# Kernel optimization log

Hardware: AMD Instinct MI355X
Metric: run time of the kernel (lower is better)

## Reference

```python
import jax, jax.numpy as jnp
import numpy as np

B = 8; A = 9; NUM_CLASSES = 80
BRANCH_HW = [(80, 80), (40, 40)]; STRIDES = [8, 16]
IMG_H, IMG_W = 640, 640
CLASS_OFFSETS = [0, 0]
SCORE_THR = 0.05; NMS_THR = 0.5; MARGIN = 0.0
PRE_NMS = 1000; POST_NMS = 300
MIN_H, MIN_W = 0.0, 0.0
BBOX_CLIP = float(np.log(1000.0 / 16.0))  # torchvision-style dw/dh clamp


def _make_anchors(H, W, stride):
    # A square anchors per cell, grid-aligned (x1,y1,x2,y2)
    sizes = np.array([16., 32., 64., 20., 40., 80., 24., 48., 96.])[:A]
    cx = (np.arange(W) + 0.5) * stride
    cy = (np.arange(H) + 0.5) * stride
    cy_g, cx_g = np.meshgrid(cy, cx, indexing='ij')  # [H,W]
    half = sizes / 2.0  # [A]
    x1 = cx_g[..., None] - half; y1 = cy_g[..., None] - half
    x2 = cx_g[..., None] + half; y2 = cy_g[..., None] + half
    anc = np.stack([x1, y1, x2, y2], -1).astype(np.float32)  # [H,W,A,4]
    anc = anc.reshape(H, W, A * 4).transpose(2, 0, 1)  # [A*4,H,W]
    return jnp.asarray(np.broadcast_to(anc[None], (B,) + anc.shape).copy())


def setup_inputs() -> dict:
    key = jax.random.key(0)
    ks = jax.random.split(key, 2)
    out = {}
    for i, (Hh, Ww) in enumerate(BRANCH_HW):
        d = jax.random.normal(ks[i], (B, Hh, Ww, A, 4 + NUM_CLASSES), jnp.float32)
        d = d.at[..., :4].multiply(0.25)  # keep box deltas in a sane range
        out['data%d' % i] = d.reshape(B, Hh, Ww, A * (4 + NUM_CLASSES)).transpose(0, 3, 1, 2)
        out['anchors%d' % i] = _make_anchors(Hh, Ww, STRIDES[i])
    return out


def _unfold(t, d):
    b = t.shape[0]
    return jnp.transpose(t, (0, 2, 3, 1)).reshape(b, -1, d)


def _decode(deltas, anchors):
    # BoxCoder((1,1,1,1)).decode_single
    aw = anchors[..., 2] - anchors[..., 0]; ah = anchors[..., 3] - anchors[..., 1]
    acx = anchors[..., 0] + 0.5 * aw; acy = anchors[..., 1] + 0.5 * ah
    dx, dy, dw, dh = (deltas[..., 0], deltas[..., 1], deltas[..., 2], deltas[..., 3])
    pcx = dx * aw + acx; pcy = dy * ah + acy
    pw = jnp.exp(jnp.minimum(dw, BBOX_CLIP)) * aw
    ph = jnp.exp(jnp.minimum(dh, BBOX_CLIP)) * ah
    return jnp.stack([pcx - 0.5 * pw, pcy - 0.5 * ph, pcx + 0.5 * pw, pcy + 0.5 * ph], -1)


def _iou(b):
    area = (b[:, 2] - b[:, 0]) * (b[:, 3] - b[:, 1])
    lt = jnp.maximum(b[:, None, :2], b[None, :, :2])
    rb = jnp.minimum(b[:, None, 2:], b[None, :, 2:])
    wh = jnp.clip(rb - lt, 0.0)
    inter = wh[..., 0] * wh[..., 1]
    return inter / (area[:, None] + area[None, :] - inter + 1e-9)


def _nms_single(boxes, cls, scores):
    # sort by score, take pre_nms_top_k
    sc, idx = jax.lax.top_k(scores, PRE_NMS)
    b = boxes[idx]; c = cls[idx]
    # score threshold + min-hw validity filter (masked instead of dynamic slice)
    valid = (sc >= SCORE_THR) & (b[:, 0] < b[:, 2] - MIN_W) & (b[:, 1] < b[:, 3] - MIN_H)
    iou = _iou(b)  # [PRE,PRE]
    rng = jnp.arange(PRE_NMS)

    def body(i, keep):
        # box j suppressed by kept box i if IoU>thr and score_i - score_j > margin
        sup = keep[i] & (iou[i] > NMS_THR) & ((sc[i] - sc) > MARGIN) & (rng > i)
        return keep & (~sup)

    keep = jax.lax.fori_loop(0, PRE_NMS, body, valid)
    # kept boxes first (score order preserved), then pad_zero to POST_NMS
    order = jnp.argsort(jnp.where(keep, rng, rng + PRE_NMS))[:POST_NMS]
    km = keep[order]
    return (jnp.where(km[:, None], b[order], 0.0),
            jnp.where(km, sc[order], 0.0),
            jnp.where(km, c[order], 0.0))


def reference(data0, data1, anchors0, anchors1):
    datas = [data0, data1]; ancs = [anchors0, anchors1]
    fa, deltas, scores, offs = [], [], [], []
    for i in range(2):
        fa.append(_unfold(ancs[i], 4))
        u = _unfold(datas[i], 4 + NUM_CLASSES)
        deltas.append(u[..., :4]); scores.append(u[..., 4:])
        offs.append(jnp.full((1, u.shape[1]), float(CLASS_OFFSETS[i]), jnp.float32))
    fa = jnp.concatenate(fa, 1); deltas = jnp.concatenate(deltas, 1)
    scores = jnp.concatenate(scores, 1); offs = jnp.concatenate(offs, 1)
    max_sc = scores.max(-1)
    cls = jnp.argmax(scores, -1).astype(jnp.float32) + offs
    boxes = _decode(deltas, fa)
    # clip to image
    x = jnp.clip(boxes[..., 0::2], 0.0, float(IMG_W))
    y = jnp.clip(boxes[..., 1::2], 0.0, float(IMG_H))
    boxes = jnp.stack([x[..., 0], y[..., 0], x[..., 1], y[..., 1]], -1)
    return jax.vmap(_nms_single)(boxes, cls, max_sc)  # ([B,POST,4],[B,POST],[B,POST])
```

## Files before the change

### kernel.cpp

```cpp
#include <hip/hip_runtime.h>
#include <math.h>

#pragma clang fp contract(off)

#define BB      8
#define AA      9
#define NCLS    80
#define NTOT    72000
#define PRE     1000
#define POST    300
#define CAP     4096
#define BCLIP   4.135166556742356f

__device__ __constant__ float c_sizes[9] = {16.f,32.f,64.f,20.f,40.f,80.f,24.f,48.f,96.f};

__device__ inline unsigned fkey(float s) {
    unsigned u = __float_as_uint(s);
    return (u & 0x80000000u) ? ~u : (u | 0x80000000u);
}

template<int BR>
__device__ inline void fused_impl(int bx, const float* __restrict__ data,
    float* __restrict__ boxes, float* __restrict__ scores, float* __restrict__ cls,
    unsigned* __restrict__ chist, unsigned* lh)
{
    constexpr int ROWF4  = BR ? 400 : 1600;
    constexpr int W      = BR ? 40 : 80;
    constexpr int STRIDE = BR ? 16 : 8;
    constexpr int NQ     = BR ? 2 : 8;

    int slab = bx / NQ;
    int q    = bx - slab * NQ;
    int b = slab / 9, a = slab - (slab / 9) * 9;
    int tid = threadIdx.x;
    bool act = tid < 200;

    const float4* d4 = (const float4*)data;
    size_t rowbase = (size_t)(b * 756 + a * 84) * ROWF4 + q * 200;

    if (act) {
        float4 del[4];
        #pragma unroll
        for (int u = 0; u < 4; u++)
            del[u] = d4[rowbase + (size_t)u * ROWF4 + tid];

        float best[4];
        int   bc[4];
        #pragma unroll
        for (int k = 0; k < 4; k++) { best[k] = -INFINITY; bc[k] = 0; }

        for (int c0 = 4; c0 < 84; c0 += 8) {
            float4 v[8];
            #pragma unroll
            for (int u = 0; u < 8; u++)
                v[u] = d4[rowbase + (size_t)(c0 + u) * ROWF4 + tid];
            #pragma unroll
            for (int u = 0; u < 8; u++) {
                int c = c0 + u - 4;
                float s0[4];
                *(float4*)s0 = v[u];
                #pragma unroll
                for (int k = 0; k < 4; k++)
                    if (s0[k] > best[k]) { best[k] = s0[k]; bc[k] = c; }
            }
        }

        float sz = c_sizes[a];
        float dx[4], dy[4], dwv[4], dhv[4];
        *(float4*)dx  = del[0];
        *(float4*)dy  = del[1];
        *(float4*)dwv = del[2];
        *(float4*)dhv = del[3];

        int ml0 = q * 800 + tid * 4;
        size_t obase = (size_t)b * NTOT + (BR ? (57600 + a * 1600) : (a * 6400));

        #pragma unroll
        for (int k = 0; k < 4; k++) {
            int hw = ml0 + k;
            int h = hw / W, w = hw - h * W;
            float cy = (h + 0.5f) * (float)STRIDE;
            float cx = (w + 0.5f) * (float)STRIDE;
            float pcx = dx[k] * sz + cx;
            float pcy = dy[k] * sz + cy;
            float pw  = expf(fminf(dwv[k], BCLIP)) * sz;
            float ph  = expf(fminf(dhv[k], BCLIP)) * sz;
            float x1 = fminf(fmaxf(pcx - 0.5f * pw, 0.f), 640.f);
            float y1 = fminf(fmaxf(pcy - 0.5f * ph, 0.f), 640.f);
            float x2 = fminf(fmaxf(pcx + 0.5f * pw, 0.f), 640.f);
            float y2 = fminf(fmaxf(pcy + 0.5f * ph, 0.f), 640.f);
            size_t o = obase + hw;
            ((float4*)boxes)[o] = make_float4(x1, y1, x2, y2);
            scores[o] = best[k];
            cls[o]    = (float)bc[k];
            atomicAdd(&lh[fkey(best[k]) >> 24], 1u);
        }
    }
    __syncthreads();
    if (lh[tid]) atomicAdd(&chist[b * 256 + tid], lh[tid]);
}

__global__ __launch_bounds__(256) void k_fused(
    const float* __restrict__ data0, const float* __restrict__ data1,
    float* __restrict__ boxes, float* __restrict__ scores, float* __restrict__ cls,
    unsigned* __restrict__ chist)
{
    __shared__ unsigned lh[256];
    lh[threadIdx.x] = 0;
    __syncthreads();
    int bx = blockIdx.x;
    if (bx < 576) fused_impl<0>(bx, data0, boxes, scores, cls, chist, lh);
    else          fused_impl<1>(bx - 576, data1, boxes, scores, cls, chist, lh);
}

__global__ __launch_bounds__(256) void k_fine(const float* __restrict__ scores,
                                              const unsigned* __restrict__ chist,
                                              unsigned* __restrict__ fhist)
{
    __shared__ unsigned S[256];
    __shared__ unsigned lh[256];
    __shared__ unsigned sC;
    int tid = threadIdx.x, b = blockIdx.y;
    S[tid]  = chist[b * 256 + tid];
    lh[tid] = 0;
    __syncthreads();
    for (int off = 1; off < 256; off <<= 1) {
        unsigned v = S[tid] + ((tid + off < 256) ? S[tid + off] : 0u);
        __syncthreads();
        S[tid] = v;
        __syncthreads();
    }
    if (S[tid] >= (unsigned)PRE && (tid == 255 || S[tid + 1] < (unsigned)PRE)) sC = tid;
    __syncthreads();
    unsigned C = sC;

    int m4 = blockIdx.x * 256 + tid;
    if (m4 < NTOT / 4) {
        float sv[4];
        *(float4*)sv = ((const float4*)(scores + (size_t)b * NTOT))[m4];
        #pragma unroll
        for (int k = 0; k < 4; k++) {
            unsigned u = fkey(sv[k]);
            if ((u >> 24) == C) atomicAdd(&lh[(u >> 16) & 0xFF], 1u);
        }
    }
    __syncthreads();
    if (lh[tid]) atomicAdd(&fhist[b * 256 + tid], lh[tid]);
}

__global__ __launch_bounds__(256) void k_compact(const float* __restrict__ scores,
                                                 const unsigned* __restrict__ chist,
                                                 const unsigned* __restrict__ fhist,
                                                 unsigned* __restrict__ cnt,
                                                 unsigned long long* __restrict__ cand)
{
    __shared__ unsigned S[256];
    __shared__ unsigned sC, sCa, sT;
    int tid = threadIdx.x, b = blockIdx.y;

    S[tid] = chist[b * 256 + tid];
    __syncthreads();
    for (int off = 1; off < 256; off <<= 1) {
        unsigned v = S[tid] + ((tid + off < 256) ? S[tid + off] : 0u);
        __syncthreads();
        S[tid] = v;
        __syncthreads();
    }
    if (S[tid] >= (unsigned)PRE && (tid == 255 || S[tid + 1] < (unsigned)PRE)) {
        sC  = tid;
        sCa = (tid == 255) ? 0u : S[tid + 1];
    }
    __syncthreads();
    unsigned C = sC, ca = sCa;
    S[tid] = fhist[b * 256 + tid];
    __syncthreads();
    for (int off = 1; off < 256; off <<= 1) {
        unsigned v = S[tid] + ((tid + off < 256) ? S[tid + off] : 0u);
        __syncthreads();
        S[tid] = v;
        __syncthreads();
    }
    if (ca + S[tid] >= (unsigned)PRE && (tid == 255 || ca + S[tid + 1] < (unsigned)PRE))
        sT = (C << 8) | (unsigned)tid;
    __syncthreads();
    unsigned Tb = sT;

    int m4 = blockIdx.x * 256 + tid;
    if (m4 >= NTOT / 4) return;
    float sv[4];
    *(float4*)sv = ((const float4*)(scores + (size_t)b * NTOT))[m4];
    #pragma unroll
    for (int k = 0; k < 4; k++) {
        unsigned u = fkey(sv[k]);
        if ((u >> 16) >= Tb) {
            int m = m4 * 4 + k;
            int n;
            if (m < 57600) { int a = m / 6400; int hw = m - a * 6400; n = hw * 9 + a; }
            else { int mm = m - 57600; int a = mm / 1600; int hw = mm - a * 1600; n = 57600 + hw * 9 + a; }
            unsigned pos = atomicAdd(&cnt[b], 1u);
            if (pos < CAP)
                cand[(size_t)b * CAP + pos] = ((unsigned long long)u << 32) | (unsigned)(~(unsigned)n);
        }
    }
}

__global__ __launch_bounds__(1024) void k_sort(
    const unsigned long long* __restrict__ cand, const unsigned* __restrict__ cnt,
    const float* __restrict__ boxes, const float* __restrict__ scores, const float* __restrict__ cls,
    float* __restrict__ sboxes, float* __restrict__ sscores, float* __restrict__ scls)
{
    __shared__ unsigned long long keys[CAP];
    int b = blockIdx.x, tid = threadIdx.x;
    int c = min((int)cnt[b], CAP);
    int P = 1024;
    while (P < c) P <<= 1;
    for (int i = tid; i < P; i += 1024)
        keys[i] = (i < c) ? cand[(size_t)b * CAP + i] : 0ULL;

    for (int k2 = 2; k2 <= P; k2 <<= 1)
        for (int j = k2 >> 1; j > 0; j >>= 1) {
            __syncthreads();
            for (int i = tid; i < P; i += 1024) {
                int l = i ^ j;
                if (l > i) {
                    unsigned long long x = keys[i], y = keys[l];
                    bool up = ((i & k2) == 0);
                    if ((x > y) == up) { keys[i] = y; keys[l] = x; }
                }
            }
        }
    __syncthreads();

    if (tid < PRE) {
        unsigned long long key = keys[P - 1 - tid];
        int n = (int)~(unsigned)(key & 0xFFFFFFFFu);
        int m;
        if (n < 57600) { int hw = n / 9; int a = n - hw * 9; m = a * 6400 + hw; }
        else { int n2 = n - 57600; int hw = n2 / 9; int a = n2 - hw * 9; m = 57600 + a * 1600 + hw; }
        size_t src = (size_t)b * NTOT + m;
        ((float4*)sboxes)[b * 1024 + tid] = ((const float4*)boxes)[src];
        sscores[b * 1024 + tid] = scores[src];
        scls[b * 1024 + tid] = cls[src];
    }
}

__global__ __launch_bounds__(1024) void k_mask(const float* __restrict__ sboxes,
                                               const float* __restrict__ sscores,
                                               unsigned long long* __restrict__ maskT)
{
    __shared__ float4 bx[64];
    __shared__ float  sl[64];
    int b = blockIdx.y, w = blockIdx.x, tid = threadIdx.x;
    if (tid < 64) {
        int i = w * 64 + tid;
        bx[tid] = ((const float4*)sboxes)[b * 1024 + i];
        sl[tid] = sscores[b * 1024 + i];
    }
    __syncthreads();
    int j = tid;
    unsigned long long* dst = &maskT[((size_t)(b * 16) + w) * 1024 + j];
    if (j >= PRE || w * 64 >= j) { *dst = 0ULL; return; }

    float4 bj = ((const float4*)sboxes)[b * 1024 + j];
    float sj = sscores[b * 1024 + j];
    float areaj = (bj.z - bj.x) * (bj.w - bj.y);
    unsigned long long bits = 0;
    int iend = min(64, j - w * 64);
    for (int ii = 0; ii < iend; ii++) {
        float4 bi = bx[ii];
        float ix1 = fmaxf(bi.x, bj.x), iy1 = fmaxf(bi.y, bj.y);
        float ix2 = fminf(bi.z, bj.z), iy2 = fminf(bi.w, bj.w);
        float iw = fmaxf(ix2 - ix1, 0.f), ih = fmaxf(iy2 - iy1, 0.f);
        float inter = iw * ih;
        float areai = (bi.z - bi.x) * (bi.w - bi.y);
        float iou = inter / (areai + areaj - inter + 1e-9f);
        if (iou > 0.5f && sl[ii] > sj) bits |= 1ull << ii;
    }
    *dst = bits;
}

__global__ __launch_bounds__(64) void k_nms(const unsigned long long* __restrict__ maskT,
                                            const float* __restrict__ sboxes,
                                            const float* __restrict__ sscores,
                                            const float* __restrict__ scls,
                                            float* __restrict__ out)
{
    int b = blockIdx.x, lane = threadIdx.x;
    const unsigned long long* base = maskT + (size_t)b * 16 * 1024;

    unsigned validbits = 0;
    #pragma unroll
    for (int c = 0; c < 16; c++) {
        int r = c * 64 + lane;
        bool v = false;
        if (r < PRE) {
            float sc = sscores[b * 1024 + r];
            float4 bbx = ((const float4*)sboxes)[b * 1024 + r];
            v = (sc >= 0.05f) && (bbx.x < bbx.z) && (bbx.y < bbx.w);
        }
        validbits |= (v ? 1u : 0u) << c;
    }

    unsigned long long keptw[16];
    #pragma unroll
    for (int c = 0; c < 16; c++) {
        unsigned long long acc = 0, col = 0;
        #pragma unroll
        for (int w = 0; w <= c; w++) {
            unsigned long long m = base[(w << 10) + c * 64 + lane];
            if (w < c) acc |= m & keptw[w];
            else       col = m;
        }
        bool alive = (((validbits >> c) & 1u) != 0u) && (acc == 0ULL);

        unsigned long long ab = __ballot(alive);
        unsigned long long kw = 0;
        while (ab) {
            int f = __ffsll((unsigned long long)ab) - 1;
            kw |= 1ULL << f;
            alive = alive && (lane != f) && (((col >> f) & 1ULL) == 0ULL);
            ab = __ballot(alive);
        }
        keptw[c] = kw;
    }

    __shared__ unsigned long long kws[16];
    __shared__ int pfx[17];
    if (lane == 0) {
        int s = 0;
        #pragma unroll
        for (int w = 0; w < 16; w++) {
            kws[w] = keptw[w];
            pfx[w] = s;
            s += __popcll(keptw[w]);
        }
        pfx[16] = s;
    }
    __syncthreads();
    int nk = pfx[16];

    float* ob = out;
    float* os = out + BB * POST * 4;
    float* oc = os + BB * POST;

    for (int r = lane; r < PRE; r += 64) {
        int w = r >> 6;
        unsigned long long kw = kws[w];
        if ((kw >> (r & 63)) & 1ULL) {
            int rank = pfx[w] + __popcll(kw & ((1ULL << (r & 63)) - 1ULL));
            if (rank < POST) {
                ((float4*)ob)[b * POST + rank] = ((const float4*)sboxes)[b * 1024 + r];
                os[b * POST + rank] = sscores[b * 1024 + r];
                oc[b * POST + rank] = scls[b * 1024 + r];
            }
        }
    }
    for (int p = nk + lane; p < POST; p += 64) {
        ((float4*)ob)[b * POST + p] = make_float4(0.f, 0.f, 0.f, 0.f);
        os[b * POST + p] = 0.f;
        oc[b * POST + p] = 0.f;
    }
}

extern "C" void kernel_launch(void* const* d_in, const int* in_sizes, int n_in,
                              void* d_out, int out_size, void* d_ws, size_t ws_size,
                              hipStream_t stream)
{
    const float* data0 = (const float*)d_in[0];
    const float* data1 = (const float*)d_in[2];
    for (int i = 0; i < n_in; i++) {
        if (in_sizes[i] == 8 * 756 * 6400) data0 = (const float*)d_in[i];
        else if (in_sizes[i] == 8 * 756 * 1600) data1 = (const float*)d_in[i];
    }

    char* ws = (char*)d_ws;
    size_t off = 0;
    auto alloc = [&](size_t bytes) -> char* {
        char* p = ws + off;
        off = (off + bytes + 255) & ~(size_t)255;
        return p;
    };

    float* boxes   = (float*)alloc((size_t)BB * NTOT * 4 * 4);
    float* scores  = (float*)alloc((size_t)BB * NTOT * 4);
    float* cls     = (float*)alloc((size_t)BB * NTOT * 4);
    unsigned* cnt   = (unsigned*)alloc(BB * 4);
    unsigned* chist = (unsigned*)alloc(BB * 256 * 4);
    unsigned* fhist = (unsigned*)alloc(BB * 256 * 4);
    unsigned long long* cand = (unsigned long long*)alloc((size_t)BB * CAP * 8);
    float* sboxes  = (float*)alloc((size_t)BB * 1024 * 4 * 4);
    float* sscores = (float*)alloc((size_t)BB * 1024 * 4);
    float* scls    = (float*)alloc((size_t)BB * 1024 * 4);
    unsigned long long* maskT = (unsigned long long*)alloc((size_t)BB * 16 * 1024 * 8);

    (void)hipMemsetAsync(cnt, 0, 256 + 2 * (size_t)BB * 256 * 4, stream);

    k_fused<<<720, 256, 0, stream>>>(data0, data1, boxes, scores, cls, chist);

    dim3 gf((NTOT / 4 + 255) / 256, BB);
    k_fine<<<gf, 256, 0, stream>>>(scores, chist, fhist);

    k_compact<<<gf, 256, 0, stream>>>(scores, chist, fhist, cnt, cand);

    k_sort<<<BB, 1024, 0, stream>>>(cand, cnt, boxes, scores, cls, sboxes, sscores, scls);

    dim3 g5(16, BB);
    k_mask<<<g5, 1024, 0, stream>>>(sboxes, sscores, maskT);

    k_nms<<<BB, 64, 0, stream>>>(maskT, sboxes, sscores, scls, (float*)d_out);
}
```

Baseline: 438.6 us.

## Decode boxes only for selected candidates and fuse sort, mask and NMS kernels

Box decoding is removed from the full-map pass and done only for the top-1000 candidates, reading deltas straight from the input tensors. The two-pass radix histogram becomes a single 16-bit global histogram built in the fused pass, with a small threshold kernel replacing the fine-histogram pass over all scores. The sort, IoU mask and NMS kernels are merged into one per-batch block that keeps boxes in shared memory. This cuts full-size box writes, one full score rescan and several launches, at the cost of a larger global histogram with contended atomics, a larger memset, and only 8 blocks doing the mask computation.

```diff
diff --git a/kernel.cpp b/kernel.cpp
--- a/kernel.cpp
+++ b/kernel.cpp
@@ -18,111 +18,82 @@
     unsigned u = __float_as_uint(s);
     return (u & 0x80000000u) ? ~u : (u | 0x80000000u);
 }
+__device__ inline float unfkey(unsigned u) {
+    return __uint_as_float((u & 0x80000000u) ? (u ^ 0x80000000u) : ~u);
+}
 
 template<int BR>
 __device__ inline void fused_impl(int bx, const float* __restrict__ data,
-    float* __restrict__ boxes, float* __restrict__ scores, float* __restrict__ cls,
-    unsigned* __restrict__ chist, unsigned* lh)
+    float* __restrict__ scores, float* __restrict__ cls,
+    unsigned* __restrict__ fhist16)
 {
     constexpr int ROWF4  = BR ? 400 : 1600;
-    constexpr int W      = BR ? 40 : 80;
-    constexpr int STRIDE = BR ? 16 : 8;
     constexpr int NQ     = BR ? 2 : 8;
 
     int slab = bx / NQ;
     int q    = bx - slab * NQ;
     int b = slab / 9, a = slab - (slab / 9) * 9;
     int tid = threadIdx.x;
-    bool act = tid < 200;
+    if (tid >= 200) return;
 
     const float4* d4 = (const float4*)data;
     size_t rowbase = (size_t)(b * 756 + a * 84) * ROWF4 + q * 200;
 
-    if (act) {
-        float4 del[4];
-        #pragma unroll
-        for (int u = 0; u < 4; u++)
-            del[u] = d4[rowbase + (size_t)u * ROWF4 + tid];
-
-        float best[4];
-        int   bc[4];
-        #pragma unroll
-        for (int k = 0; k < 4; k++) { best[k] = -INFINITY; bc[k] = 0; }
-
-        for (int c0 = 4; c0 < 84; c0 += 8) {
-            float4 v[8];
+    float best[4];
+    int   bc[4];
+    #pragma unroll
+    for (int k = 0; k < 4; k++) { best[k] = -INFINITY; bc[k] = 0; }
+
+    for (int c0 = 4; c0 < 84; c0 += 8) {
+        float4 v[8];
+        #pragma unroll
+        for (int u = 0; u < 8; u++)
+            v[u] = d4[rowbase + (size_t)(c0 + u) * ROWF4 + tid];
+        #pragma unroll
+        for (int u = 0; u < 8; u++) {
+            int c = c0 + u - 4;
+            float s0[4];
+            *(float4*)s0 = v[u];
             #pragma unroll
-            for (int u = 0; u < 8; u++)
-                v[u] = d4[rowbase + (size_t)(c0 + u) * ROWF4 + tid];
-            #pragma unroll
-            for (int u = 0; u < 8; u++) {
-                int c = c0 + u - 4;
-                float s0[4];
-                *(float4*)s0 = v[u];
-                #pragma unroll
-                for (int k = 0; k < 4; k++)
-                    if (s0[k] > best[k]) { best[k] = s0[k]; bc[k] = c; }
-            }
-        }
-
-        float sz = c_sizes[a];
-        float dx[4], dy[4], dwv[4], dhv[4];
-        *(float4*)dx  = del[0];
-        *(float4*)dy  = del[1];
-        *(float4*)dwv = del[2];
-        *(float4*)dhv = del[3];
-
-        int ml0 = q * 800 + tid * 4;
-        size_t obase = (size_t)b * NTOT + (BR ? (57600 + a * 1600) : (a * 6400));
-
-        #pragma unroll
-        for (int k = 0; k < 4; k++) {
-            int hw = ml0 + k;
-            int h = hw / W, w = hw - h * W;
-            float cy = (h + 0.5f) * (float)STRIDE;
-            float cx = (w + 0.5f) * (float)STRIDE;
-            float pcx = dx[k] * sz + cx;
-            float pcy = dy[k] * sz + cy;
-            float pw  = expf(fminf(dwv[k], BCLIP)) * sz;
-            float ph  = expf(fminf(dhv[k], BCLIP)) * sz;
-            float x1 = fminf(fmaxf(pcx - 0.5f * pw, 0.f), 640.f);
-            float y1 = fminf(fmaxf(pcy - 0.5f * ph, 0.f), 640.f);
-            float x2 = fminf(fmaxf(pcx + 0.5f * pw, 0.f), 640.f);
-            float y2 = fminf(fmaxf(pcy + 0.5f * ph, 0.f), 640.f);
-            size_t o = obase + hw;
-            ((float4*)boxes)[o] = make_float4(x1, y1, x2, y2);
-            scores[o] = best[k];
-            cls[o]    = (float)bc[k];
-            atomicAdd(&lh[fkey(best[k]) >> 24], 1u);
-        }
-    }
-    __syncthreads();
-    if (lh[tid]) atomicAdd(&chist[b * 256 + tid], lh[tid]);
+            for (int k = 0; k < 4; k++)
+                if (s0[k] > best[k]) { best[k] = s0[k]; bc[k] = c; }
+        }
+    }
+
+    int ml0 = q * 800 + tid * 4;
+    size_t obase = (size_t)b * NTOT + (BR ? (57600 + a * 1600) : (a * 6400));
+    size_t o4 = (obase + ml0) >> 2;
+    ((float4*)scores)[o4] = make_float4(best[0], best[1], best[2], best[3]);
+    ((float4*)cls)[o4]    = make_float4((float)bc[0], (float)bc[1],
+                                        (float)bc[2], (float)bc[3]);
+    unsigned* hb = fhist16 + (size_t)b * 65536;
+    #pragma unroll
+    for (int k = 0; k < 4; k++)
+        atomicAdd(&hb[fkey(best[k]) >> 16], 1u);
 }
 
 __global__ __launch_bounds__(256) void k_fused(
     const float* __restrict__ data0, const float* __restrict__ data1,
-    float* __restrict__ boxes, float* __restrict__ scores, float* __restrict__ cls,
-    unsigned* __restrict__ chist)
-{
-    __shared__ unsigned lh[256];
-    lh[threadIdx.x] = 0;
-    __syncthreads();
+    float* __restrict__ scores, float* __restrict__ cls,
+    unsigned* __restrict__ fhist16)
+{
     int bx = blockIdx.x;
-    if (bx < 576) fused_impl<0>(bx, data0, boxes, scores, cls, chist, lh);
-    else          fused_impl<1>(bx - 576, data1, boxes, scores, cls, chist, lh);
-}
-
-__global__ __launch_bounds__(256) void k_fine(const float* __restrict__ scores,
-                                              const unsigned* __restrict__ chist,
-                                              unsigned* __restrict__ fhist)
+    if (bx < 576) fused_impl<0>(bx, data0, scores, cls, fhist16);
+    else          fused_impl<1>(bx - 576, data1, scores, cls, fhist16);
+}
+
+__global__ __launch_bounds__(256) void k_thr(const unsigned* __restrict__ fhist16,
+                                             unsigned* __restrict__ T)
 {
     __shared__ unsigned S[256];
-    __shared__ unsigned lh[256];
-    __shared__ unsigned sC;
-    int tid = threadIdx.x, b = blockIdx.y;
-    S[tid]  = chist[b * 256 + tid];
-    lh[tid] = 0;
+    __shared__ unsigned sC, sCa;
+    int b = blockIdx.x, tid = threadIdx.x;
+
+    const uint4* h4 = (const uint4*)(fhist16 + (size_t)b * 65536 + tid * 256);
+    unsigned s = 0;
+    #pragma unroll 8
+    for (int i = 0; i < 64; i++) { uint4 v = h4[i]; s += v.x + v.y + v.z + v.w; }
+    S[tid] = s;
     __syncthreads();
     for (int off = 1; off < 256; off <<= 1) {
         unsigned v = S[tid] + ((tid + off < 256) ? S[tid + off] : 0u);
@@ -130,35 +101,14 @@
         S[tid] = v;
         __syncthreads();
     }
-    if (S[tid] >= (unsigned)PRE && (tid == 255 || S[tid + 1] < (unsigned)PRE)) sC = tid;
-    __syncthreads();
-    unsigned C = sC;
-
-    int m4 = blockIdx.x * 256 + tid;
-    if (m4 < NTOT / 4) {
-        float sv[4];
-        *(float4*)sv = ((const float4*)(scores + (size_t)b * NTOT))[m4];
-        #pragma unroll
-        for (int k = 0; k < 4; k++) {
-            unsigned u = fkey(sv[k]);
-            if ((u >> 24) == C) atomicAdd(&lh[(u >> 16) & 0xFF], 1u);
-        }
-    }
-    __syncthreads();
-    if (lh[tid]) atomicAdd(&fhist[b * 256 + tid], lh[tid]);
-}
-
-__global__ __launch_bounds__(256) void k_compact(const float* __restrict__ scores,
-                                                 const unsigned* __restrict__ chist,
-                                                 const unsigned* __restrict__ fhist,
-                                                 unsigned* __restrict__ cnt,
-                                                 unsigned long long* __restrict__ cand)
-{
-    __shared__ unsigned S[256];
-    __shared__ unsigned sC, sCa, sT;
-    int tid = threadIdx.x, b = blockIdx.y;
-
-    S[tid] = chist[b * 256 + tid];
+    if (S[tid] >= (unsigned)PRE && (tid == 255 || S[tid + 1] < (unsigned)PRE)) {
+        sC  = tid;
+        sCa = (tid == 255) ? 0u : S[tid + 1];
+    }
+    __syncthreads();
+    unsigned C = sC, ca = sCa;
+
+    S[tid] = fhist16[(size_t)b * 65536 + C * 256 + tid];
     __syncthreads();
     for (int off = 1; off < 256; off <<= 1) {
         unsigned v = S[tid] + ((tid + off < 256) ? S[tid + off] : 0u);
@@ -166,29 +116,21 @@
         S[tid] = v;
         __syncthreads();
     }
-    if (S[tid] >= (unsigned)PRE && (tid == 255 || S[tid + 1] < (unsigned)PRE)) {
-        sC  = tid;
-        sCa = (tid == 255) ? 0u : S[tid + 1];
-    }
-    __syncthreads();
-    unsigned C = sC, ca = sCa;
-    S[tid] = fhist[b * 256 + tid];
-    __syncthreads();
-    for (int off = 1; off < 256; off <<= 1) {
-        unsigned v = S[tid] + ((tid + off < 256) ? S[tid + off] : 0u);
-        __syncthreads();
-        S[tid] = v;
-        __syncthreads();
-    }
     if (ca + S[tid] >= (unsigned)PRE && (tid == 255 || ca + S[tid + 1] < (unsigned)PRE))
-        sT = (C << 8) | (unsigned)tid;
-    __syncthreads();
-    unsigned Tb = sT;
-
-    int m4 = blockIdx.x * 256 + tid;
+        T[b] = C * 256 + (unsigned)tid;
+}
+
+__global__ __launch_bounds__(256) void k_compact(const float* __restrict__ scores,
+                                                 const unsigned* __restrict__ T,
+                                                 unsigned* __restrict__ cnt,
+                                                 unsigned long long* __restrict__ cand)
+{
+    int m4 = blockIdx.x * 256 + threadIdx.x;
+    int b = blockIdx.y;
     if (m4 >= NTOT / 4) return;
     float sv[4];
     *(float4*)sv = ((const float4*)(scores + (size_t)b * NTOT))[m4];
+    unsigned Tb = T[b];
     #pragma unroll
     for (int k = 0; k < 4; k++) {
         unsigned u = fkey(sv[k]);
@@ -204,13 +146,20 @@
     }
 }
 
-__global__ __launch_bounds__(1024) void k_sort(
+__global__ __launch_bounds__(1024) void k_select(
     const unsigned long long* __restrict__ cand, const unsigned* __restrict__ cnt,
-    const float* __restrict__ boxes, const float* __restrict__ scores, const float* __restrict__ cls,
-    float* __restrict__ sboxes, float* __restrict__ sscores, float* __restrict__ scls)
+    const float* __restrict__ cls,
+    const float* __restrict__ data0, const float* __restrict__ data1,
+    unsigned long long* __restrict__ maskT, float* __restrict__ out)
 {
     __shared__ unsigned long long keys[CAP];
+    __shared__ float4 sbx[1024];
+    __shared__ float  ssc[1024];
+    __shared__ float  scl[1024];
+    __shared__ unsigned long long kws[16];
+
     int b = blockIdx.x, tid = threadIdx.x;
+
     int c = min((int)cnt[b], CAP);
     int P = 1024;
     while (P < c) P <<= 1;
@@ -234,131 +183,147 @@
     if (tid < PRE) {
         unsigned long long key = keys[P - 1 - tid];
         int n = (int)~(unsigned)(key & 0xFFFFFFFFu);
-        int m;
-        if (n < 57600) { int hw = n / 9; int a = n - hw * 9; m = a * 6400 + hw; }
-        else { int n2 = n - 57600; int hw = n2 / 9; int a = n2 - hw * 9; m = 57600 + a * 1600 + hw; }
-        size_t src = (size_t)b * NTOT + m;
-        ((float4*)sboxes)[b * 1024 + tid] = ((const float4*)boxes)[src];
-        sscores[b * 1024 + tid] = scores[src];
-        scls[b * 1024 + tid] = cls[src];
-    }
-}
-
-__global__ __launch_bounds__(1024) void k_mask(const float* __restrict__ sboxes,
-                                               const float* __restrict__ sscores,
-                                               unsigned long long* __restrict__ maskT)
-{
-    __shared__ float4 bx[64];
-    __shared__ float  sl[64];
-    int b = blockIdx.y, w = blockIdx.x, tid = threadIdx.x;
+        int a, hw, W, STRIDE, m;
+        const float* dsrc;
+        size_t rstride;
+        if (n < 57600) {
+            hw = n / 9; a = n - hw * 9; m = a * 6400 + hw;
+            W = 80; STRIDE = 8; dsrc = data0; rstride = 6400;
+        } else {
+            int n2 = n - 57600;
+            hw = n2 / 9; a = n2 - hw * 9; m = 57600 + a * 1600 + hw;
+            W = 40; STRIDE = 16; dsrc = data1; rstride = 1600;
+        }
+        size_t dbase = (size_t)(b * 756 + a * 84) * rstride + hw;
+        float dx = dsrc[dbase];
+        float dy = dsrc[dbase + rstride];
+        float dw = dsrc[dbase + 2 * rstride];
+        float dh = dsrc[dbase + 3 * rstride];
+
+        float sz = c_sizes[a];
+        int h = hw / W, w = hw - h * W;
+        float cy = (h + 0.5f) * (float)STRIDE;
+        float cx = (w + 0.5f) * (float)STRIDE;
+        float pcx = dx * sz + cx;
+        float pcy = dy * sz + cy;
+        float pw  = expf(fminf(dw, BCLIP)) * sz;
+        float ph  = expf(fminf(dh, BCLIP)) * sz;
+        float x1 = fminf(fmaxf(pcx - 0.5f * pw, 0.f), 640.f);
+        float y1 = fminf(fmaxf(pcy - 0.5f * ph, 0.f), 640.f);
+        float x2 = fminf(fmaxf(pcx + 0.5f * pw, 0.f), 640.f);
+        float y2 = fminf(fmaxf(pcy + 0.5f * ph, 0.f), 640.f);
+
+        sbx[tid] = make_float4(x1, y1, x2, y2);
+        ssc[tid] = unfkey((unsigned)(key >> 32));
+        scl[tid] = cls[(size_t)b * NTOT + m];
+    } else {
+        sbx[tid] = make_float4(0.f, 0.f, 0.f, 0.f);
+        ssc[tid] = 0.f;
+        scl[tid] = 0.f;
+    }
+    __syncthreads();
+
+    unsigned long long* maskTb = maskT + (size_t)b * 16 * 1024;
+    {
+        int j = tid;
+        float4 bj = sbx[j];
+        float sj = ssc[j];
+        float areaj = (bj.z - bj.x) * (bj.w - bj.y);
+        #pragma unroll
+        for (int w = 0; w < 16; w++) {
+            unsigned long long bits = 0;
+            if (j < PRE && w * 64 < j) {
+                int iend = min(64, j - w * 64);
+                for (int ii = 0; ii < iend; ii++) {
+                    float4 bi = sbx[w * 64 + ii];
+                    float ix1 = fmaxf(bi.x, bj.x), iy1 = fmaxf(bi.y, bj.y);
+                    float ix2 = fminf(bi.z, bj.z), iy2 = fminf(bi.w, bj.w);
+                    float iw = fmaxf(ix2 - ix1, 0.f), ih = fmaxf(iy2 - iy1, 0.f);
+                    float inter = iw * ih;
+                    float areai = (bi.z - bi.x) * (bi.w - bi.y);
+                    float iou = inter / (areai + areaj - inter + 1e-9f);
+                    if (iou > 0.5f && ssc[w * 64 + ii] > sj) bits |= 1ull << ii;
+                }
+            }
+            maskTb[(w << 10) + j] = bits;
+        }
+    }
+    __syncthreads();
+
     if (tid < 64) {
-        int i = w * 64 + tid;
-        bx[tid] = ((const float4*)sboxes)[b * 1024 + i];
-        sl[tid] = sscores[b * 1024 + i];
-    }
-    __syncthreads();
-    int j = tid;
-    unsigned long long* dst = &maskT[((size_t)(b * 16) + w) * 1024 + j];
-    if (j >= PRE || w * 64 >= j) { *dst = 0ULL; return; }
-
-    float4 bj = ((const float4*)sboxes)[b * 1024 + j];
-    float sj = sscores[b * 1024 + j];
-    float areaj = (bj.z - bj.x) * (bj.w - bj.y);
-    unsigned long long bits = 0;
-    int iend = min(64, j - w * 64);
-    for (int ii = 0; ii < iend; ii++) {
-        float4 bi = bx[ii];
-        float ix1 = fmaxf(bi.x, bj.x), iy1 = fmaxf(bi.y, bj.y);
-        float ix2 = fminf(bi.z, bj.z), iy2 = fminf(bi.w, bj.w);
-        float iw = fmaxf(ix2 - ix1, 0.f), ih = fmaxf(iy2 - iy1, 0.f);
-        float inter = iw * ih;
-        float areai = (bi.z - bi.x) * (bi.w - bi.y);
-        float iou = inter / (areai + areaj - inter + 1e-9f);
-        if (iou > 0.5f && sl[ii] > sj) bits |= 1ull << ii;
-    }
-    *dst = bits;
-}
-
-__global__ __launch_bounds__(64) void k_nms(const unsigned long long* __restrict__ maskT,
-                                            const float* __restrict__ sboxes,
-                                            const float* __restrict__ sscores,
-                                            const float* __restrict__ scls,
-                                            float* __restrict__ out)
-{
-    int b = blockIdx.x, lane = threadIdx.x;
-    const unsigned long long* base = maskT + (size_t)b * 16 * 1024;
-
-    unsigned validbits = 0;
-    #pragma unroll
-    for (int c = 0; c < 16; c++) {
-        int r = c * 64 + lane;
-        bool v = false;
-        if (r < PRE) {
-            float sc = sscores[b * 1024 + r];
-            float4 bbx = ((const float4*)sboxes)[b * 1024 + r];
-            v = (sc >= 0.05f) && (bbx.x < bbx.z) && (bbx.y < bbx.w);
-        }
-        validbits |= (v ? 1u : 0u) << c;
-    }
-
-    unsigned long long keptw[16];
-    #pragma unroll
-    for (int c = 0; c < 16; c++) {
-        unsigned long long acc = 0, col = 0;
-        #pragma unroll
-        for (int w = 0; w <= c; w++) {
-            unsigned long long m = base[(w << 10) + c * 64 + lane];
-            if (w < c) acc |= m & keptw[w];
-            else       col = m;
-        }
-        bool alive = (((validbits >> c) & 1u) != 0u) && (acc == 0ULL);
-
-        unsigned long long ab = __ballot(alive);
-        unsigned long long kw = 0;
-        while (ab) {
-            int f = __ffsll((unsigned long long)ab) - 1;
-            kw |= 1ULL << f;
-            alive = alive && (lane != f) && (((col >> f) & 1ULL) == 0ULL);
-            ab = __ballot(alive);
-        }
-        keptw[c] = kw;
-    }
-
-    __shared__ unsigned long long kws[16];
-    __shared__ int pfx[17];
-    if (lane == 0) {
-        int s = 0;
-        #pragma unroll
-        for (int w = 0; w < 16; w++) {
-            kws[w] = keptw[w];
-            pfx[w] = s;
-            s += __popcll(keptw[w]);
-        }
-        pfx[16] = s;
-    }
-    __syncthreads();
-    int nk = pfx[16];
+        int lane = tid;
+        unsigned validbits = 0;
+        #pragma unroll
+        for (int cc = 0; cc < 16; cc++) {
+            int r = cc * 64 + lane;
+            bool v = false;
+            if (r < PRE) {
+                float sc = ssc[r];
+                float4 bbx = sbx[r];
+                v = (sc >= 0.05f) && (bbx.x < bbx.z) && (bbx.y < bbx.w);
+            }
+            validbits |= (v ? 1u : 0u) << cc;
+        }
+
+        unsigned long long keptw[16];
+        #pragma unroll
+        for (int cc = 0; cc < 16; cc++) {
+            unsigned long long acc = 0, col = 0;
+            #pragma unroll
+            for (int w = 0; w <= cc; w++) {
+                unsigned long long m = maskTb[(w << 10) + cc * 64 + lane];
+                if (w < cc) acc |= m & keptw[w];
+                else        col = m;
+            }
+            bool alive = (((validbits >> cc) & 1u) != 0u) && (acc == 0ULL);
+
+            unsigned long long ab = __ballot(alive);
+            unsigned long long kw = 0;
+            while (ab) {
+                int f = __ffsll((unsigned long long)ab) - 1;
+                kw |= 1ULL << f;
+                alive = alive && (lane != f) && (((col >> f) & 1ULL) == 0ULL);
+                ab = __ballot(alive);
+            }
+            keptw[cc] = kw;
+        }
+        if (lane == 0) {
+            #pragma unroll
+            for (int w = 0; w < 16; w++) kws[w] = keptw[w];
+        }
+    }
+    __syncthreads();
 
     float* ob = out;
     float* os = out + BB * POST * 4;
     float* oc = os + BB * POST;
 
-    for (int r = lane; r < PRE; r += 64) {
-        int w = r >> 6;
-        unsigned long long kw = kws[w];
-        if ((kw >> (r & 63)) & 1ULL) {
-            int rank = pfx[w] + __popcll(kw & ((1ULL << (r & 63)) - 1ULL));
-            if (rank < POST) {
-                ((float4*)ob)[b * POST + rank] = ((const float4*)sboxes)[b * 1024 + r];
-                os[b * POST + rank] = sscores[b * 1024 + r];
-                oc[b * POST + rank] = scls[b * 1024 + r];
-            }
-        }
-    }
-    for (int p = nk + lane; p < POST; p += 64) {
-        ((float4*)ob)[b * POST + p] = make_float4(0.f, 0.f, 0.f, 0.f);
-        os[b * POST + p] = 0.f;
-        oc[b * POST + p] = 0.f;
+    int nk = 0;
+    {
+        int w = tid >> 6;
+        int rank = 0;
+        #pragma unroll
+        for (int ww = 0; ww < 16; ww++) {
+            int p = __popcll(kws[ww]);
+            if (ww < w) rank += p;
+            nk += p;
+        }
+        if (tid < PRE) {
+            unsigned long long kw = kws[w];
+            if ((kw >> (tid & 63)) & 1ULL) {
+                rank += __popcll(kw & ((1ULL << (tid & 63)) - 1ULL));
+                if (rank < POST) {
+                    ((float4*)ob)[b * POST + rank] = sbx[tid];
+                    os[b * POST + rank] = ssc[tid];
+                    oc[b * POST + rank] = scl[tid];
+                }
+            }
+        }
+    }
+    if (tid >= nk && tid < POST) {
+        ((float4*)ob)[b * POST + tid] = make_float4(0.f, 0.f, 0.f, 0.f);
+        os[b * POST + tid] = 0.f;
+        oc[b * POST + tid] = 0.f;
     }
 }
 
@@ -381,31 +346,23 @@
         return p;
     };
 
-    float* boxes   = (float*)alloc((size_t)BB * NTOT * 4 * 4);
     float* scores  = (float*)alloc((size_t)BB * NTOT * 4);
     float* cls     = (float*)alloc((size_t)BB * NTOT * 4);
-    unsigned* cnt   = (unsigned*)alloc(BB * 4);
-    unsigned* chist = (unsigned*)alloc(BB * 256 * 4);
-    unsigned* fhist = (unsigned*)alloc(BB * 256 * 4);
-    unsigned long long* cand = (unsigned long long*)alloc((size_t)BB * CAP * 8);
-    float* sboxes  = (float*)alloc((size_t)BB * 1024 * 4 * 4);
-    float* sscores = (float*)alloc((size_t)BB * 1024 * 4);
-    float* scls    = (float*)alloc((size_t)BB * 1024 * 4);
+    unsigned* cnt     = (unsigned*)alloc(BB * 4);
+    unsigned* fhist16 = (unsigned*)alloc((size_t)BB * 65536 * 4);
+    unsigned* T    = (unsigned*)alloc(BB * 4);
+    unsigned long long* cand  = (unsigned long long*)alloc((size_t)BB * CAP * 8);
     unsigned long long* maskT = (unsigned long long*)alloc((size_t)BB * 16 * 1024 * 8);
 
-    (void)hipMemsetAsync(cnt, 0, 256 + 2 * (size_t)BB * 256 * 4, stream);
-
-    k_fused<<<720, 256, 0, stream>>>(data0, data1, boxes, scores, cls, chist);
+    (void)hipMemsetAsync(cnt, 0, 256 + (size_t)BB * 65536 * 4, stream);
+
+    k_fused<<<720, 256, 0, stream>>>(data0, data1, scores, cls, fhist16);
+
+    k_thr<<<BB, 256, 0, stream>>>(fhist16, T);
 
     dim3 gf((NTOT / 4 + 255) / 256, BB);
-    k_fine<<<gf, 256, 0, stream>>>(scores, chist, fhist);
-
-    k_compact<<<gf, 256, 0, stream>>>(scores, chist, fhist, cnt, cand);
-
-    k_sort<<<BB, 1024, 0, stream>>>(cand, cnt, boxes, scores, cls, sboxes, sscores, scls);
-
-    dim3 g5(16, BB);
-    k_mask<<<g5, 1024, 0, stream>>>(sboxes, sscores, maskT);
-
-    k_nms<<<BB, 64, 0, stream>>>(maskT, sboxes, sscores, scls, (float*)d_out);
-}
+    k_compact<<<gf, 256, 0, stream>>>(scores, T, cnt, cand);
+
+    k_select<<<BB, 1024, 0, stream>>>(cand, cnt, cls, data0, data1, maskT,
+                                      (float*)d_out);
+}
```

New measurement: 702.0 us. 60.1% more time.

## Decode boxes lazily for top-K candidates only in sort kernel

Applied to the files above, without the earlier changes.

Box decoding moves out of the fused scan kernel, which no longer reads delta rows or writes a full boxes buffer for all 72000 anchors per image. The sort kernel instead reads the four deltas from the raw inputs for just the top 1000 survivors and decodes them there. Each such load is a scattered gather. The score is recovered from the sort key instead of being reloaded, and the fused kernel now writes scores and classes as float4 stores.

```diff
diff --git a/kernel.cpp b/kernel.cpp
--- a/kernel.cpp
+++ b/kernel.cpp
@@ -18,31 +18,26 @@
     unsigned u = __float_as_uint(s);
     return (u & 0x80000000u) ? ~u : (u | 0x80000000u);
 }
+__device__ inline float unfkey(unsigned u) {
+    return __uint_as_float((u & 0x80000000u) ? (u ^ 0x80000000u) : ~u);
+}
 
 template<int BR>
 __device__ inline void fused_impl(int bx, const float* __restrict__ data,
-    float* __restrict__ boxes, float* __restrict__ scores, float* __restrict__ cls,
+    float* __restrict__ scores, float* __restrict__ cls,
     unsigned* __restrict__ chist, unsigned* lh)
 {
     constexpr int ROWF4  = BR ? 400 : 1600;
-    constexpr int W      = BR ? 40 : 80;
-    constexpr int STRIDE = BR ? 16 : 8;
     constexpr int NQ     = BR ? 2 : 8;
 
     int slab = bx / NQ;
     int q    = bx - slab * NQ;
     int b = slab / 9, a = slab - (slab / 9) * 9;
     int tid = threadIdx.x;
-    bool act = tid < 200;
-
-    const float4* d4 = (const float4*)data;
-    size_t rowbase = (size_t)(b * 756 + a * 84) * ROWF4 + q * 200;
-
-    if (act) {
-        float4 del[4];
-        #pragma unroll
-        for (int u = 0; u < 4; u++)
-            del[u] = d4[rowbase + (size_t)u * ROWF4 + tid];
+
+    if (tid < 200) {
+        const float4* d4 = (const float4*)data;
+        size_t rowbase = (size_t)(b * 756 + a * 84) * ROWF4 + q * 200;
 
         float best[4];
         int   bc[4];
@@ -65,52 +60,31 @@
             }
         }
 
-        float sz = c_sizes[a];
-        float dx[4], dy[4], dwv[4], dhv[4];
-        *(float4*)dx  = del[0];
-        *(float4*)dy  = del[1];
-        *(float4*)dwv = del[2];
-        *(float4*)dhv = del[3];
-
         int ml0 = q * 800 + tid * 4;
         size_t obase = (size_t)b * NTOT + (BR ? (57600 + a * 1600) : (a * 6400));
-
+        size_t o4 = (obase + ml0) >> 2;
+        ((float4*)scores)[o4] = make_float4(best[0], best[1], best[2], best[3]);
+        ((float4*)cls)[o4]    = make_float4((float)bc[0], (float)bc[1],
+                                            (float)bc[2], (float)bc[3]);
         #pragma unroll
-        for (int k = 0; k < 4; k++) {
-            int hw = ml0 + k;
-            int h = hw / W, w = hw - h * W;
-            float cy = (h + 0.5f) * (float)STRIDE;
-            float cx = (w + 0.5f) * (float)STRIDE;
-            float pcx = dx[k] * sz + cx;
-            float pcy = dy[k] * sz + cy;
-            float pw  = expf(fminf(dwv[k], BCLIP)) * sz;
-            float ph  = expf(fminf(dhv[k], BCLIP)) * sz;
-            float x1 = fminf(fmaxf(pcx - 0.5f * pw, 0.f), 640.f);
-            float y1 = fminf(fmaxf(pcy - 0.5f * ph, 0.f), 640.f);
-            float x2 = fminf(fmaxf(pcx + 0.5f * pw, 0.f), 640.f);
-            float y2 = fminf(fmaxf(pcy + 0.5f * ph, 0.f), 640.f);
-            size_t o = obase + hw;
-            ((float4*)boxes)[o] = make_float4(x1, y1, x2, y2);
-            scores[o] = best[k];
-            cls[o]    = (float)bc[k];
+        for (int k = 0; k < 4; k++)
             atomicAdd(&lh[fkey(best[k]) >> 24], 1u);
-        }
-    }
-    __syncthreads();
-    if (lh[tid]) atomicAdd(&chist[b * 256 + tid], lh[tid]);
+    }
+    __syncthreads();
+    if (lh[threadIdx.x]) atomicAdd(&chist[b * 256 + threadIdx.x], lh[threadIdx.x]);
 }
 
 __global__ __launch_bounds__(256) void k_fused(
     const float* __restrict__ data0, const float* __restrict__ data1,
-    float* __restrict__ boxes, float* __restrict__ scores, float* __restrict__ cls,
+    float* __restrict__ scores, float* __restrict__ cls,
     unsigned* __restrict__ chist)
 {
     __shared__ unsigned lh[256];
     lh[threadIdx.x] = 0;
     __syncthreads();
     int bx = blockIdx.x;
-    if (bx < 576) fused_impl<0>(bx, data0, boxes, scores, cls, chist, lh);
-    else          fused_impl<1>(bx - 576, data1, boxes, scores, cls, chist, lh);
+    if (bx < 576) fused_impl<0>(bx, data0, scores, cls, chist, lh);
+    else          fused_impl<1>(bx - 576, data1, scores, cls, chist, lh);
 }
 
 __global__ __launch_bounds__(256) void k_fine(const float* __restrict__ scores,
@@ -206,7 +180,8 @@
 
 __global__ __launch_bounds__(1024) void k_sort(
     const unsigned long long* __restrict__ cand, const unsigned* __restrict__ cnt,
-    const float* __restrict__ boxes, const float* __restrict__ scores, const float* __restrict__ cls,
+    const float* __restrict__ cls,
+    const float* __restrict__ data0, const float* __restrict__ data1,
     float* __restrict__ sboxes, float* __restrict__ sscores, float* __restrict__ scls)
 {
     __shared__ unsigned long long keys[CAP];
@@ -234,13 +209,39 @@
     if (tid < PRE) {
         unsigned long long key = keys[P - 1 - tid];
         int n = (int)~(unsigned)(key & 0xFFFFFFFFu);
-        int m;
-        if (n < 57600) { int hw = n / 9; int a = n - hw * 9; m = a * 6400 + hw; }
-        else { int n2 = n - 57600; int hw = n2 / 9; int a = n2 - hw * 9; m = 57600 + a * 1600 + hw; }
-        size_t src = (size_t)b * NTOT + m;
-        ((float4*)sboxes)[b * 1024 + tid] = ((const float4*)boxes)[src];
-        sscores[b * 1024 + tid] = scores[src];
-        scls[b * 1024 + tid] = cls[src];
+        int a, hw, W, STRIDE, m;
+        const float* dsrc;
+        size_t rstride;
+        if (n < 57600) {
+            hw = n / 9; a = n - hw * 9; m = a * 6400 + hw;
+            W = 80; STRIDE = 8; dsrc = data0; rstride = 6400;
+        } else {
+            int n2 = n - 57600;
+            hw = n2 / 9; a = n2 - hw * 9; m = 57600 + a * 1600 + hw;
+            W = 40; STRIDE = 16; dsrc = data1; rstride = 1600;
+        }
+        size_t dbase = (size_t)(b * 756 + a * 84) * rstride + hw;
+        float dx = dsrc[dbase];
+        float dy = dsrc[dbase + rstride];
+        float dw = dsrc[dbase + 2 * rstride];
+        float dh = dsrc[dbase + 3 * rstride];
+
+        float sz = c_sizes[a];
+        int h = hw / W, w = hw - h * W;
+        float cy = (h + 0.5f) * (float)STRIDE;
+        float cx = (w + 0.5f) * (float)STRIDE;
+        float pcx = dx * sz + cx;
+        float pcy = dy * sz + cy;
+        float pw  = expf(fminf(dw, BCLIP)) * sz;
+        float ph  = expf(fminf(dh, BCLIP)) * sz;
+        float x1 = fminf(fmaxf(pcx - 0.5f * pw, 0.f), 640.f);
+        float y1 = fminf(fmaxf(pcy - 0.5f * ph, 0.f), 640.f);
+        float x2 = fminf(fmaxf(pcx + 0.5f * pw, 0.f), 640.f);
+        float y2 = fminf(fmaxf(pcy + 0.5f * ph, 0.f), 640.f);
+
+        ((float4*)sboxes)[b * 1024 + tid] = make_float4(x1, y1, x2, y2);
+        sscores[b * 1024 + tid] = unfkey((unsigned)(key >> 32));
+        scls[b * 1024 + tid] = cls[(size_t)b * NTOT + m];
     }
 }
 
@@ -381,7 +382,6 @@
         return p;
     };
 
-    float* boxes   = (float*)alloc((size_t)BB * NTOT * 4 * 4);
     float* scores  = (float*)alloc((size_t)BB * NTOT * 4);
     float* cls     = (float*)alloc((size_t)BB * NTOT * 4);
     unsigned* cnt   = (unsigned*)alloc(BB * 4);
@@ -395,14 +395,15 @@
 
     (void)hipMemsetAsync(cnt, 0, 256 + 2 * (size_t)BB * 256 * 4, stream);
 
-    k_fused<<<720, 256, 0, stream>>>(data0, data1, boxes, scores, cls, chist);
+    k_fused<<<720, 256, 0, stream>>>(data0, data1, scores, cls, chist);
 
     dim3 gf((NTOT / 4 + 255) / 256, BB);
     k_fine<<<gf, 256, 0, stream>>>(scores, chist, fhist);
 
     k_compact<<<gf, 256, 0, stream>>>(scores, chist, fhist, cnt, cand);
 
-    k_sort<<<BB, 1024, 0, stream>>>(cand, cnt, boxes, scores, cls, sboxes, sscores, scls);
+    k_sort<<<BB, 1024, 0, stream>>>(cand, cnt, cls, data0, data1,
+                                    sboxes, sscores, scls);
 
     dim3 g5(16, BB);
     k_mask<<<g5, 1024, 0, stream>>>(sboxes, sscores, maskT);
```

After: 442.4 us. No clear change (+0.9%).
